# Performance work log

Hardware: AMD Instinct MI355X
Metric: run time of the kernel (lower is better)

Reference implementation:

```python
import jax, jax.numpy as jnp
import numpy as np

B, S, H = 1, 2048, 1024
NH, HD = 16, 64
WIN = 512
M_MEM, M_PER = 512, 64
SCALE = 1.0 / np.sqrt(HD)
NEG_INF = jnp.float32(-1e30)


def setup_inputs() -> dict:
    key = jax.random.key(0)
    ks = jax.random.split(key, 22)
    std = 1.0 / np.sqrt(H)
    def w(k):
        return (jax.random.normal(k, (H, H), jnp.float32) * std)
    names = ['local_wq','local_wk','local_wv','local_wo',
             'long_wq','long_wk','long_wv','long_wo',
             'mem_wq','mem_wk','mem_wv','mem_wo',
             'per_wq','per_wk','per_wv','per_wo']
    d = {n: w(ks[i]) for i, n in enumerate(names)}
    d['gate_w'] = jax.random.normal(ks[16], (4 * H, 4), jnp.float32) * 0.02
    d['gate_b'] = jnp.zeros((4,), jnp.float32)
    d['x'] = jax.random.normal(ks[17], (B, S, H), jnp.float32)
    d['memory_kv'] = jax.random.normal(ks[18], (B, M_MEM, H), jnp.float32)
    d['persona_kv'] = jax.random.normal(ks[19], (B, M_PER, H), jnp.float32)
    return d


def _split_heads(t):
    # (B, T, H) -> (B, NH, T, HD)
    b, t_, _ = t.shape
    return t.reshape(b, t_, NH, HD).transpose(0, 2, 1, 3)


def _merge_heads(t):
    b, h, t_, d = t.shape
    return t.transpose(0, 2, 1, 3).reshape(b, t_, h * d)


def _self_attn(x, wq, wk, wv, wo, mask):
    # mask: (S, S) bool, True = masked out
    q = _split_heads(x @ wq)
    k = _split_heads(x @ wk)
    v = _split_heads(x @ wv)
    scores = jnp.einsum('bhsd,bhtd->bhst', q, k) * SCALE
    scores = jnp.where(mask[None, None], NEG_INF, scores)
    a = jax.nn.softmax(scores, axis=-1)
    out = jnp.einsum('bhst,bhtd->bhsd', a, v)
    return _merge_heads(out) @ wo


def _cross_attn(x, ctx, wq, wk, wv, wo):
    q = _split_heads(x @ wq)
    k = _split_heads(ctx @ wk)
    v = _split_heads(ctx @ wv)
    scores = jnp.einsum('bhsd,bhmd->bhsm', q, k) * SCALE
    a = jax.nn.softmax(scores, axis=-1)
    out = jnp.einsum('bhsm,bhmd->bhsd', a, v)
    return _merge_heads(out) @ wo


def reference(x, memory_kv, persona_kv,
              local_wq, local_wk, local_wv, local_wo,
              long_wq, long_wk, long_wv, long_wo,
              mem_wq, mem_wk, mem_wv, mem_wo,
              per_wq, per_wk, per_wv, per_wo,
              gate_w, gate_b):
    s = x.shape[1]
    idx = jnp.arange(s)
    causal = idx[None, :] > idx[:, None]                    # future tokens masked
    local = causal | ((idx[:, None] - idx[None, :]) > WIN)  # sliding window + causal

    local_out = _self_attn(x, local_wq, local_wk, local_wv, local_wo, local)
    long_out = _self_attn(x, long_wq, long_wk, long_wv, long_wo, causal)
    mem_out = _cross_attn(x, memory_kv, mem_wq, mem_wk, mem_wv, mem_wo)
    per_out = _cross_attn(x, persona_kv, per_wq, per_wk, per_wv, per_wo)

    outs = (local_out, long_out, mem_out, per_out)
    gate_in = jnp.concatenate(outs, axis=-1)                # (B, S, 4H)
    gates = jax.nn.softmax(gate_in @ gate_w + gate_b, axis=-1)  # (B, S, 4)
    fused = sum(gates[..., i:i + 1] * o for i, o in enumerate(outs))
    return fused  # emotion_scale = 1.0, dropout off (eval)
```

## Files before the change

kernel.cpp:

```cpp
#include <hip/hip_runtime.h>

#define S 2048
#define H 1024
#define NH 16
#define HD 64
#define WIN 512
#define SCALE_Q 0.18033688f
#define SM_SHIFT 16.0f

typedef unsigned short u16;
typedef unsigned int u32;
typedef __attribute__((ext_vector_type(8))) short bfrag;
typedef __attribute__((ext_vector_type(4))) float facc;
typedef __attribute__((ext_vector_type(4))) unsigned short u16x4;

constexpr size_t M1    = 1u << 20;
constexpr size_t WTO   = 0;
constexpr size_t XBO   = 8 * M1;
constexpr size_t MEMBO = 10 * M1;
constexpr size_t PERBO = MEMBO + (M1 >> 1);
constexpr size_t QO    = PERBO + (M1 >> 4);
constexpr size_t KVO   = QO + 8 * M1;
constexpr size_t K2O   = KVO + 8 * M1;
constexpr size_t V2O   = K2O + (M1 >> 1);
constexpr size_t K3O   = V2O + (M1 >> 1);
constexpr size_t V3O   = K3O + (M1 >> 4);
constexpr size_t VT1O  = V3O + (M1 >> 4);
constexpr size_t VT2O  = VT1O + 2 * M1;
constexpr size_t VT3O  = VT2O + (M1 >> 1);
constexpr size_t RECSZ = 8704;

__device__ __forceinline__ u16 f2bf(float f) {
    union { float f; unsigned u; } v; v.f = f;
    unsigned r = v.u + 0x7fffu + ((v.u >> 16) & 1u);
    return (u16)(r >> 16);
}
__device__ __forceinline__ float bf2f(u16 b) {
    union { unsigned u; float f; } v; v.u = ((unsigned)b) << 16;
    return v.f;
}
__device__ __forceinline__ void gload16(const u16* g, u16* l) {
    __builtin_amdgcn_global_load_lds(
        (const __attribute__((address_space(1))) u32*)g,
        (__attribute__((address_space(3))) u32*)l, 16, 0, 0);
}
__device__ __forceinline__ u32 cvt_pk(float a, float b) {
    u32 w;
    asm("v_cvt_pk_bf16_f32 %0, %1, %2" : "=v"(w) : "v"(a), "v"(b));
    return w;
}

__global__ __launch_bounds__(256)
void cast_all(const float* __restrict__ x, const float* __restrict__ mem,
              const float* __restrict__ per, u16* __restrict__ ws) {
    int i = blockIdx.x * 256 + threadIdx.x;
    const float* src; u16* dst;
    if (i < 262144)           { src = x;   dst = ws + XBO;   }
    else if (i < 327680)      { src = mem; dst = ws + MEMBO; i -= 262144; }
    else if (i < 335872)      { src = per; dst = ws + PERBO; i -= 327680; }
    else return;
    const float4* p = reinterpret_cast<const float4*>(src) + (size_t)i * 2;
    float4 a = p[0], b = p[1];
    u16x4 o0, o1;
    o0[0] = f2bf(a.x); o0[1] = f2bf(a.y); o0[2] = f2bf(a.z); o0[3] = f2bf(a.w);
    o1[0] = f2bf(b.x); o1[1] = f2bf(b.y); o1[2] = f2bf(b.z); o1[3] = f2bf(b.w);
    u16x4* q = reinterpret_cast<u16x4*>(dst) + (size_t)i * 2;
    q[0] = o0; q[1] = o1;
}

__global__ __launch_bounds__(256)
void transp_cast(const float* __restrict__ w0, const float* __restrict__ w1,
                 const float* __restrict__ w2, const float* __restrict__ w3,
                 u16* __restrict__ wt) {
    __shared__ float t[64][65];
    const float* w = blockIdx.z == 0 ? w0 : blockIdx.z == 1 ? w1
                   : blockIdx.z == 2 ? w2 : w3;
    u16* o = wt + (size_t)blockIdx.z * (1024 * 1024);
    const int kt = blockIdx.y * 64, nt = blockIdx.x * 64;
    const int r = threadIdx.x >> 4, c4 = (threadIdx.x & 15) * 4;
#pragma unroll
    for (int p = 0; p < 4; p++) {
        float4 v = *reinterpret_cast<const float4*>(
            &w[(size_t)(kt + r + p * 16) * 1024 + nt + c4]);
        t[r + p * 16][c4 + 0] = v.x; t[r + p * 16][c4 + 1] = v.y;
        t[r + p * 16][c4 + 2] = v.z; t[r + p * 16][c4 + 3] = v.w;
    }
    __syncthreads();
#pragma unroll
    for (int p = 0; p < 4; p++) {
        int nn = r + p * 16;
        u16x4 ov;
        ov[0] = f2bf(t[c4 + 0][nn]); ov[1] = f2bf(t[c4 + 1][nn]);
        ov[2] = f2bf(t[c4 + 2][nn]); ov[3] = f2bf(t[c4 + 3][nn]);
        *reinterpret_cast<u16x4*>(&o[(size_t)(nt + nn) * 1024 + kt + c4]) = ov;
    }
}

__global__ __launch_bounds__(256)
void transp_v(u16* __restrict__ ws) {
    const int z = blockIdx.z;
    const int Skv = (z < 2) ? 2048 : (z == 2 ? 512 : 64);
    const int kb = blockIdx.x;
    if (kb * 64 >= Skv) return;
    const int h = blockIdx.y;
    const u16* V = ws + (z == 0 ? KVO + 2 * M1 : z == 1 ? KVO + 6 * M1
                       : z == 2 ? V2O : V3O);
    u16* VT = ws + (z == 0 ? XBO : z == 1 ? VT1O : z == 2 ? VT2O : VT3O);
    __shared__ __align__(16) u16 t[64][72];
    {
        const int r = threadIdx.x >> 3, c8 = (threadIdx.x & 7) * 8;
#pragma unroll
        for (int p = 0; p < 2; p++) {
            int rr = r + p * 32;
            bfrag v = *reinterpret_cast<const bfrag*>(
                &V[(size_t)(kb * 64 + rr) * 1024 + h * 64 + c8]);
            *reinterpret_cast<bfrag*>(&t[rr][c8]) = v;
        }
    }
    __syncthreads();
    {
        const int d = threadIdx.x & 63;
        const int k8b = (threadIdx.x >> 6) * 8;
#pragma unroll
        for (int p = 0; p < 2; p++) {
            int k8 = k8b + p * 32;
            bfrag o;
#pragma unroll
            for (int j = 0; j < 8; j++) o[j] = (short)t[k8 + j][d];
            *reinterpret_cast<bfrag*>(
                &VT[(size_t)(h * 64 + d) * Skv + kb * 64 + k8]) = o;
        }
    }
}

__global__ __launch_bounds__(256)
void gemm_bf16(const u16* __restrict__ A, const u16* __restrict__ Bt,
               u16* __restrict__ C, int M, long sA, long sB, long sC,
               int scaleMask) {
    __shared__ __align__(16) u16 sa[128 * 64];
    __shared__ __align__(16) u16 sb[128 * 64];
    A  += (size_t)blockIdx.z * sA;
    Bt += (size_t)blockIdx.z * sB;
    C  += (size_t)blockIdx.z * sC;
    const float scl = ((scaleMask >> blockIdx.z) & 1) ? SCALE_Q : 1.0f;
    const int tid = threadIdx.x;
    const int wid = tid >> 6, lane = tid & 63;
    const int lhi = lane >> 4, llo = lane & 15;
    const int wm = wid >> 1, wn = wid & 1;
    const int row0 = blockIdx.y * 128, col0 = blockIdx.x * 128;

    facc acc[4][4];
#pragma unroll
    for (int i = 0; i < 4; i++)
#pragma unroll
        for (int j = 0; j < 4; j++)
#pragma unroll
            for (int k = 0; k < 4; k++) acc[i][j][k] = 0.f;

    const int srow = lane >> 3, schunk = lane & 7;
    for (int kt = 0; kt < 16; kt++) {
        __syncthreads();
        const int k0 = kt * 64;
#pragma unroll
        for (int j = 0; j < 4; j++) {
            int r = wid * 32 + j * 8 + srow;
            int ck = schunk ^ (r & 7);
            int ar = row0 + r; if (ar > M - 1) ar = M - 1;
            gload16(&A[(size_t)ar * 1024 + k0 + ck * 8], &sa[(wid * 4 + j) * 512]);
            gload16(&Bt[(size_t)(col0 + r) * 1024 + k0 + ck * 8], &sb[(wid * 4 + j) * 512]);
        }
        __syncthreads();
#pragma unroll
        for (int ks = 0; ks < 2; ks++) {
            bfrag af[4], bfv[4];
#pragma unroll
            for (int mf = 0; mf < 4; mf++) {
                int r = wm * 64 + mf * 16 + llo;
                int p = (ks * 4 + lhi) ^ (r & 7);
                af[mf] = *reinterpret_cast<const bfrag*>(&sa[r * 64 + p * 8]);
            }
#pragma unroll
            for (int nf = 0; nf < 4; nf++) {
                int r = wn * 64 + nf * 16 + llo;
                int p = (ks * 4 + lhi) ^ (r & 7);
                bfv[nf] = *reinterpret_cast<const bfrag*>(&sb[r * 64 + p * 8]);
            }
            __builtin_amdgcn_s_setprio(1);
#pragma unroll
            for (int mf = 0; mf < 4; mf++)
#pragma unroll
                for (int nf = 0; nf < 4; nf++)
                    acc[mf][nf] = __builtin_amdgcn_mfma_f32_16x16x32_bf16(
                        af[mf], bfv[nf], acc[mf][nf], 0, 0, 0);
            __builtin_amdgcn_s_setprio(0);
        }
    }
#pragma unroll
    for (int mf = 0; mf < 4; mf++) {
#pragma unroll
        for (int r = 0; r < 4; r++) {
            int row = row0 + wm * 64 + mf * 16 + lhi * 4 + r;
            if (row < M) {
#pragma unroll
                for (int nf = 0; nf < 4; nf++) {
                    int col = col0 + wn * 64 + nf * 16 + llo;
                    C[(size_t)row * 1024 + col] = f2bf(acc[mf][nf][r] * scl);
                }
            }
        }
    }
}

__global__ __launch_bounds__(256)
void attn_tiled(u16* __restrict__ ws) {
    __shared__ __align__(16) u16 ksm[64 * 64];
    __shared__ __align__(16) u16 vtm[64 * 64];
    __shared__ __align__(16) u16 psm[4][16][72];

    const int blk = blockIdx.x;
    int branch, h, qb, pair = 0, half = 0;
    bool partial = false;
    if (blk < 256) {
        pair = blk >> 1; half = blk & 1;
        qb = 15 - (pair >> 4); h = pair & 15;
        branch = 1; partial = true;
    } else if (blk < 384) { int t = blk - 256; branch = 1; qb = 7 - (t >> 4);  h = t & 15; }
    else if (blk < 640)   { int t = blk - 384; branch = 0; qb = 15 - (t >> 4); h = t & 15; }
    else if (blk < 896)   { int t = blk - 640; branch = 2; qb = t >> 4;        h = t & 15; }
    else                  { int t = blk - 896; branch = 3; qb = t >> 4;        h = t & 15; }

    size_t kb_, vb_; int Skv, maskMode;
    if (branch == 0)      { kb_ = KVO;          vb_ = XBO;  Skv = 2048; maskMode = 2; }
    else if (branch == 1) { kb_ = KVO + 4 * M1; vb_ = VT1O; Skv = 2048; maskMode = 1; }
    else if (branch == 2) { kb_ = K2O;          vb_ = VT2O; Skv = 512;  maskMode = 0; }
    else                  { kb_ = K3O;          vb_ = VT3O; Skv = 64;   maskMode = 0; }
    const u16* Kp  = ws + kb_;
    const u16* VTp = ws + vb_;
    u16* Qp = ws + QO + (size_t)branch * 2 * M1;

    const int tid = threadIdx.x, wid = tid >> 6, lane = tid & 63;
    const int llo = lane & 15, lhi = lane >> 4;
    const int q0 = qb * 128;
    const int qw = q0 + wid * 32;
    const int hoff = h * 64;

    int tBeg, tEnd;
    if (partial) {
        int n = qb + 1;
        tBeg = half * n; tEnd = tBeg + n;
    } else {
        tEnd = maskMode ? (qb * 2 + 2) : (Skv >> 6);
        tBeg = (maskMode == 2 && q0 >= WIN) ? ((q0 - WIN) >> 6) : 0;
    }
    int myBeg = tBeg, myEnd = tEnd;
    if (maskMode) { int e = ((qw + 31) >> 6) + 1; if (e < myEnd) myEnd = e; }
    if (maskMode == 2 && qw >= WIN) { int b = (qw - WIN) >> 6; if (b > myBeg) myBeg = b; }

    bfrag qf[2][2];
#pragma unroll
    for (int sub = 0; sub < 2; sub++)
#pragma unroll
        for (int ds = 0; ds < 2; ds++)
            qf[sub][ds] = *reinterpret_cast<const bfrag*>(
                &Qp[(size_t)(qw + sub * 16 + llo) * 1024 + hoff + ds * 32 + lhi * 8]);

    facc ot[2][4];
    float lsum[2] = {0.f, 0.f};
#pragma unroll
    for (int sub = 0; sub < 2; sub++)
#pragma unroll
        for (int db = 0; db < 4; db++)
#pragma unroll
            for (int k = 0; k < 4; k++) ot[sub][db][k] = 0.f;

    const int srow = lane >> 3, schunk = lane & 7;

    for (int kt = tBeg; kt < tEnd; kt++) {
        __syncthreads();
#pragma unroll
        for (int j = 0; j < 2; j++) {
            int r = wid * 16 + j * 8 + srow;
            int ck = schunk ^ (r & 7);
            gload16(&Kp[(size_t)(kt * 64 + r) * 1024 + hoff + ck * 8],
                    &ksm[(wid * 2 + j) * 512]);
            gload16(&VTp[(size_t)(hoff + r) * Skv + kt * 64 + ck * 8],
                    &vtm[(wid * 2 + j) * 512]);
        }
        __syncthreads();

        if (kt >= myBeg && kt < myEnd) {
            bfrag kf[4][2], vf[4][2];
#pragma unroll
            for (int nf = 0; nf < 4; nf++)
#pragma unroll
                for (int ds = 0; ds < 2; ds++) {
                    int r = nf * 16 + llo;
                    int p = (ds * 4 + lhi) ^ (r & 7);
                    kf[nf][ds] = *reinterpret_cast<const bfrag*>(
                        &ksm[r * 64 + p * 8]);
                }
#pragma unroll
            for (int db = 0; db < 4; db++)
#pragma unroll
                for (int ks = 0; ks < 2; ks++) {
                    int d = db * 16 + llo;
                    int p = (ks * 4 + lhi) ^ (d & 7);
                    vf[db][ks] = *reinterpret_cast<const bfrag*>(
                        &vtm[d * 64 + p * 8]);
                }

#pragma unroll
            for (int sub = 0; sub < 2; sub++) {
                const int qsb = qw + sub * 16;
                facc st[4];
#pragma unroll
                for (int nf = 0; nf < 4; nf++)
#pragma unroll
                    for (int k = 0; k < 4; k++) st[nf][k] = 0.f;
                __builtin_amdgcn_s_setprio(1);
#pragma unroll
                for (int nf = 0; nf < 4; nf++)
#pragma unroll
                    for (int ds = 0; ds < 2; ds++)
                        st[nf] = __builtin_amdgcn_mfma_f32_16x16x32_bf16(
                            kf[nf][ds], qf[sub][ds], st[nf], 0, 0, 0);
                __builtin_amdgcn_s_setprio(0);

                float s[16];
#pragma unroll
                for (int nf = 0; nf < 4; nf++)
#pragma unroll
                    for (int r = 0; r < 4; r++) s[nf * 4 + r] = st[nf][r];

                const bool needC = maskMode && (kt * 64 + 63 > qsb);
                const bool needW = (maskMode == 2) && (kt * 64 < qsb + 15 - WIN);
                if (needC || needW) {
                    const int qi = qsb + llo;
#pragma unroll
                    for (int nf = 0; nf < 4; nf++)
#pragma unroll
                        for (int r = 0; r < 4; r++) {
                            int key = kt * 64 + nf * 16 + lhi * 4 + r;
                            if ((needC && key > qi) || (needW && (qi - key) > WIN))
                                s[nf * 4 + r] = -1e30f;
                        }
                }
                float p[16];
#pragma unroll
                for (int i = 0; i < 16; i++)
                    p[i] = __builtin_amdgcn_exp2f(s[i] - SM_SHIFT);
#pragma unroll
                for (int i = 0; i < 16; i++) lsum[sub] += p[i];

#pragma unroll
                for (int nf = 0; nf < 4; nf++)
#pragma unroll
                    for (int rp = 0; rp < 2; rp++) {
                        u32 w = cvt_pk(p[nf * 4 + rp * 2], p[nf * 4 + rp * 2 + 1]);
                        *reinterpret_cast<u32*>(
                            &psm[wid][llo][nf * 16 + lhi * 4 + rp * 2]) = w;
                    }
                bfrag pf0 = *reinterpret_cast<const bfrag*>(&psm[wid][llo][lhi * 8]);
                bfrag pf1 = *reinterpret_cast<const bfrag*>(&psm[wid][llo][32 + lhi * 8]);
                __builtin_amdgcn_s_setprio(1);
#pragma unroll
                for (int db = 0; db < 4; db++) {
                    ot[sub][db] = __builtin_amdgcn_mfma_f32_16x16x32_bf16(
                        vf[db][0], pf0, ot[sub][db], 0, 0, 0);
                    ot[sub][db] = __builtin_amdgcn_mfma_f32_16x16x32_bf16(
                        vf[db][1], pf1, ot[sub][db], 0, 0, 0);
                }
                __builtin_amdgcn_s_setprio(0);
            }
        }
    }

    if (!partial) {
#pragma unroll
        for (int sub = 0; sub < 2; sub++) {
            float l = lsum[sub];
            l += __shfl_xor(l, 16);
            l += __shfl_xor(l, 32);
            float inv = 1.f / l;
            u16* orow = &Qp[(size_t)(qw + sub * 16 + llo) * 1024 + hoff];
#pragma unroll
            for (int db = 0; db < 4; db++) {
                u16x4 pk;
#pragma unroll
                for (int r = 0; r < 4; r++) pk[r] = f2bf(ot[sub][db][r] * inv);
                *reinterpret_cast<u16x4*>(&orow[db * 16 + lhi * 4]) = pk;
            }
        }
    } else {
        float* rec = reinterpret_cast<float*>(ws) + (size_t)(pair * 2 + half) * RECSZ;
#pragma unroll
        for (int sub = 0; sub < 2; sub++) {
            float l = lsum[sub];
            l += __shfl_xor(l, 16);
            l += __shfl_xor(l, 32);
            rec[8192 + sub * 256 + tid] = l;
#pragma unroll
            for (int db = 0; db < 4; db++)
                *reinterpret_cast<facc*>(&rec[tid * 32 + sub * 16 + db * 4]) =
                    ot[sub][db];
        }
    }
}

__global__ __launch_bounds__(256)
void combine_split(u16* __restrict__ ws) {
    const int pair = blockIdx.x;
    const int qb = 15 - (pair >> 4), h = pair & 15;
    const int tid = threadIdx.x, wid = tid >> 6, lane = tid & 63;
    const int llo = lane & 15, lhi = lane >> 4;
    const float* r0 = reinterpret_cast<const float*>(ws) + (size_t)(pair * 2) * RECSZ;
    const float* r1 = r0 + RECSZ;
    u16* Qp = ws + QO + 2 * M1;
    const int qw = qb * 128 + wid * 32;
#pragma unroll
    for (int sub = 0; sub < 2; sub++) {
        float inv = 1.f / (r0[8192 + sub * 256 + tid] + r1[8192 + sub * 256 + tid]);
        u16* orow = &Qp[(size_t)(qw + sub * 16 + llo) * 1024 + h * 64];
#pragma unroll
        for (int db = 0; db < 4; db++) {
            u16x4 pk;
#pragma unroll
            for (int r = 0; r < 4; r++) {
                float v = r0[tid * 32 + sub * 16 + db * 4 + r] +
                          r1[tid * 32 + sub * 16 + db * 4 + r];
                pk[r] = f2bf(v * inv);
            }
            *reinterpret_cast<u16x4*>(&orow[db * 16 + lhi * 4]) = pk;
        }
    }
}

__global__ __launch_bounds__(256)
void gate_fuse(const u16* __restrict__ o4, const float* __restrict__ gw,
               const float* __restrict__ gb, float* __restrict__ out) {
    const int s = blockIdx.x, tid = threadIdx.x;
    const u16* ob0 = o4 + (size_t)s * H;
    float p[4] = {0.f, 0.f, 0.f, 0.f};
    for (int b = 0; b < 4; b++) {
        const u16* obb = ob0 + b * 2 * M1;
        const float* gwb = gw + (size_t)b * H * 4;
        for (int i = tid; i < H; i += 256) {
            float xv = bf2f(obb[i]);
            float4 g4 = *reinterpret_cast<const float4*>(&gwb[(size_t)i * 4]);
            p[0] += xv * g4.x; p[1] += xv * g4.y;
            p[2] += xv * g4.z; p[3] += xv * g4.w;
        }
    }
#pragma unroll
    for (int off = 1; off < 64; off <<= 1)
#pragma unroll
        for (int j = 0; j < 4; j++) p[j] += __shfl_xor(p[j], off);
    __shared__ float red[4][4];
    if ((tid & 63) == 0) {
        int w = tid >> 6;
#pragma unroll
        for (int j = 0; j < 4; j++) red[w][j] = p[j];
    }
    __syncthreads();
    float gl[4];
#pragma unroll
    for (int j = 0; j < 4; j++)
        gl[j] = gb[j] + red[0][j] + red[1][j] + red[2][j] + red[3][j];
    float mx = fmaxf(fmaxf(gl[0], gl[1]), fmaxf(gl[2], gl[3]));
    float e[4]; float tot = 0.f;
#pragma unroll
    for (int j = 0; j < 4; j++) { e[j] = __expf(gl[j] - mx); tot += e[j]; }
    float inv = 1.f / tot;
    int d = tid * 4;
    float4 rv; rv.x = rv.y = rv.z = rv.w = 0.f;
#pragma unroll
    for (int b = 0; b < 4; b++) {
        const u16* obb = ob0 + b * 2 * M1 + d;
        float wgt = e[b] * inv;
        rv.x += wgt * bf2f(obb[0]);
        rv.y += wgt * bf2f(obb[1]);
        rv.z += wgt * bf2f(obb[2]);
        rv.w += wgt * bf2f(obb[3]);
    }
    *reinterpret_cast<float4*>(&out[(size_t)s * H + d]) = rv;
}

extern "C" void kernel_launch(void* const* d_in, const int* in_sizes, int n_in,
                              void* d_out, int out_size, void* d_ws, size_t ws_size,
                              hipStream_t stream) {
    const float* Wm[16];
    for (int i = 0; i < 16; i++) Wm[i] = (const float*)d_in[i];
    const float* gw = (const float*)d_in[16];
    const float* gb = (const float*)d_in[17];
    const float* x = (const float*)d_in[18];
    const float* mem = (const float*)d_in[19];
    const float* per = (const float*)d_in[20];
    float* out = (float*)d_out;
    u16* ws = (u16*)d_ws;

    dim3 blk(256);
    cast_all<<<dim3(1312), blk, 0, stream>>>(x, mem, per, ws);

    transp_cast<<<dim3(16, 16, 4), blk, 0, stream>>>(
        Wm[0], Wm[4], Wm[8], Wm[12], ws + WTO);
    transp_cast<<<dim3(16, 16, 4), blk, 0, stream>>>(
        Wm[1], Wm[2], Wm[5], Wm[6], ws + WTO + 4 * M1);
    gemm_bf16<<<dim3(8, 16, 8), blk, 0, stream>>>(
        ws + XBO, ws + WTO, ws + QO, 2048, 0, (long)M1, (long)(2 * M1), 0xF);

    transp_cast<<<dim3(16, 16, 4), blk, 0, stream>>>(
        Wm[9], Wm[10], Wm[13], Wm[14], ws + WTO);
    gemm_bf16<<<dim3(8, 4, 2), blk, 0, stream>>>(
        ws + MEMBO, ws + WTO, ws + K2O, 512, 0, (long)M1, (long)(M1 >> 1), 0);
    gemm_bf16<<<dim3(8, 1, 2), blk, 0, stream>>>(
        ws + PERBO, ws + WTO + 2 * M1, ws + K3O, 64, 0, (long)M1, (long)(M1 >> 4), 0);

    transp_v<<<dim3(32, 16, 4), blk, 0, stream>>>(ws);
    attn_tiled<<<dim3(1152), blk, 0, stream>>>(ws);
    combine_split<<<dim3(128), blk, 0, stream>>>(ws);

    transp_cast<<<dim3(16, 16, 4), blk, 0, stream>>>(
        Wm[3], Wm[7], Wm[11], Wm[15], ws + WTO);
    gemm_bf16<<<dim3(8, 16, 4), blk, 0, stream>>>(
        ws + QO, ws + WTO, ws + KVO, 2048, (long)(2 * M1), (long)M1,
        (long)(2 * M1), 0);

    gate_fuse<<<dim3(S), blk, 0, stream>>>(ws + KVO, gw, gb, out);
}
```

Baseline: 204.6 us.

## Add double-buffered 256x256 GEMM kernel for the Q/K/V projections

Adds a new 512-thread GEMM kernel with 256x256 output tiles, double-buffered LDS staging via direct global-to-LDS loads, an XOR swizzle, and explicit vmcnt waits and barriers. It replaces the 128x128 GEMM for the eight x-projection matmuls. The larger tiles raise arithmetic intensity and the prefetch two stages ahead overlaps loads with MFMA work. In exchange it uses 128KB of LDS per block and launches only 256 blocks, so occupancy is lower and tail balance on the GPU may suffer.

```diff
diff --git a/kernel.cpp b/kernel.cpp
--- a/kernel.cpp
+++ b/kernel.cpp
@@ -48,6 +48,13 @@
     u32 w;
     asm("v_cvt_pk_bf16_f32 %0, %1, %2" : "=v"(w) : "v"(a), "v"(b));
     return w;
+}
+__device__ __forceinline__ void blockbar() {
+    __builtin_amdgcn_sched_barrier(0);
+    asm volatile("" ::: "memory");
+    __builtin_amdgcn_s_barrier();
+    asm volatile("" ::: "memory");
+    __builtin_amdgcn_sched_barrier(0);
 }
 
 __global__ __launch_bounds__(256)
@@ -133,6 +140,108 @@
     }
 }
 
+__global__ __launch_bounds__(512, 2)
+void gemm256(const u16* __restrict__ A, const u16* __restrict__ Bt,
+             u16* __restrict__ C, long sB, long sC, int scaleMask) {
+    __shared__ __align__(16) u16 sa[2][256 * 64];
+    __shared__ __align__(16) u16 sb[2][256 * 64];
+    Bt += (size_t)blockIdx.z * sB;
+    C  += (size_t)blockIdx.z * sC;
+    const float scl = ((scaleMask >> blockIdx.z) & 1) ? SCALE_Q : 1.0f;
+    const int tid = threadIdx.x;
+    const int wid = tid >> 6, lane = tid & 63;
+    const int lhi = lane >> 4, llo = lane & 15;
+    const int wm = wid >> 2, wn = wid & 3;
+    const int row0 = blockIdx.y * 256, col0 = blockIdx.x * 256;
+
+    facc acc[8][4];
+#pragma unroll
+    for (int i = 0; i < 8; i++)
+#pragma unroll
+        for (int j = 0; j < 4; j++)
+#pragma unroll
+            for (int k = 0; k < 4; k++) acc[i][j][k] = 0.f;
+
+    auto stage = [&](int s, int kt) {
+        const int k0 = kt * 64;
+#pragma unroll
+        for (int j = 0; j < 4; j++) {
+            int i = j * 512 + tid;
+            int r = i >> 3;
+            int ck = (i & 7) ^ (r & 7);
+            u16* da = &sa[s][(size_t)(j * 512 + wid * 64) * 8];
+            u16* db = &sb[s][(size_t)(j * 512 + wid * 64) * 8];
+            gload16(&A[(size_t)(row0 + r) * 1024 + k0 + ck * 8], da);
+            gload16(&Bt[(size_t)(col0 + r) * 1024 + k0 + ck * 8], db);
+        }
+    };
+
+    stage(0, 0);
+    stage(1, 1);
+    __builtin_amdgcn_sched_barrier(0);
+    asm volatile("s_waitcnt vmcnt(8)" ::: "memory");
+    blockbar();
+
+    for (int j = 0; j < 16; j++) {
+        const int sl = j & 1;
+        const u16* pa = &sa[sl][0];
+        const u16* pb = &sb[sl][0];
+        bfrag bfr[2][4];
+#pragma unroll
+        for (int ks = 0; ks < 2; ks++) {
+#pragma unroll
+            for (int mg = 0; mg < 2; mg++) {
+                bfrag af[4];
+#pragma unroll
+                for (int mf = 0; mf < 4; mf++) {
+                    int r = wm * 128 + mg * 64 + mf * 16 + llo;
+                    int p = (ks * 4 + lhi) ^ (r & 7);
+                    af[mf] = *reinterpret_cast<const bfrag*>(&pa[r * 64 + p * 8]);
+                }
+                if (mg == 0) {
+#pragma unroll
+                    for (int nf = 0; nf < 4; nf++) {
+                        int r = wn * 64 + nf * 16 + llo;
+                        int p = (ks * 4 + lhi) ^ (r & 7);
+                        bfr[ks][nf] = *reinterpret_cast<const bfrag*>(&pb[r * 64 + p * 8]);
+                    }
+                }
+                __builtin_amdgcn_s_setprio(1);
+#pragma unroll
+                for (int mf = 0; mf < 4; mf++)
+#pragma unroll
+                    for (int nf = 0; nf < 4; nf++)
+                        acc[mg * 4 + mf][nf] = __builtin_amdgcn_mfma_f32_16x16x32_bf16(
+                            af[mf], bfr[ks][nf], acc[mg * 4 + mf][nf], 0, 0, 0);
+                __builtin_amdgcn_s_setprio(0);
+                blockbar();
+            }
+        }
+        if (j + 2 < 16) {
+            stage(sl, j + 2);
+            __builtin_amdgcn_sched_barrier(0);
+            asm volatile("s_waitcnt vmcnt(8)" ::: "memory");
+            blockbar();
+        } else if (j == 14) {
+            asm volatile("s_waitcnt vmcnt(0)" ::: "memory");
+            blockbar();
+        }
+    }
+
+#pragma unroll
+    for (int mf8 = 0; mf8 < 8; mf8++) {
+#pragma unroll
+        for (int r = 0; r < 4; r++) {
+            int row = row0 + wm * 128 + mf8 * 16 + lhi * 4 + r;
+#pragma unroll
+            for (int nf = 0; nf < 4; nf++) {
+                int col = col0 + wn * 64 + nf * 16 + llo;
+                C[(size_t)row * 1024 + col] = f2bf(acc[mf8][nf][r] * scl);
+            }
+        }
+    }
+}
+
 __global__ __launch_bounds__(256)
 void gemm_bf16(const u16* __restrict__ A, const u16* __restrict__ Bt,
                u16* __restrict__ C, int M, long sA, long sB, long sC,
@@ -505,8 +614,8 @@
         Wm[0], Wm[4], Wm[8], Wm[12], ws + WTO);
     transp_cast<<<dim3(16, 16, 4), blk, 0, stream>>>(
         Wm[1], Wm[2], Wm[5], Wm[6], ws + WTO + 4 * M1);
-    gemm_bf16<<<dim3(8, 16, 8), blk, 0, stream>>>(
-        ws + XBO, ws + WTO, ws + QO, 2048, 0, (long)M1, (long)(2 * M1), 0xF);
+    gemm256<<<dim3(4, 8, 8), dim3(512), 0, stream>>>(
+        ws + XBO, ws + WTO, ws + QO, (long)M1, (long)(2 * M1), 0xF);
 
     transp_cast<<<dim3(16, 16, 4), blk, 0, stream>>>(
         Wm[9], Wm[10], Wm[13], Wm[14], ws + WTO);
```

Measured after the change: 203.1 us. No clear change (-0.7%).
